# Kernel optimization log

Measured on AMD Instinct MI355X. Metric: run time of the kernel, lower is better.

Reference implementation:

```python
import jax, jax.numpy as jnp
import numpy as np

E, B, S, D, F = 8, 2, 1024, 1024, 4096


def setup_inputs() -> dict:
    key = jax.random.key(0)
    ks = jax.random.split(key, 9)
    sc_d = 1.0 / np.sqrt(D)
    sc_f = 1.0 / np.sqrt(F)
    hidden_states = jax.random.normal(ks[0], (B, S, D), dtype=jnp.float32)
    # router outputs set externally on the parent model in the original code
    gating_probs = jax.nn.softmax(jax.random.normal(ks[1], (B, E), dtype=jnp.float32), axis=-1)
    shared_gate_prob = jax.nn.sigmoid(jax.random.normal(ks[2], (B, 1), dtype=jnp.float32))
    # stacked expert SwiGLU MLP weights (Llama-style gate/up/down)
    Wg = jax.random.normal(ks[3], (E, D, F), dtype=jnp.float32) * sc_d
    Wu = jax.random.normal(ks[4], (E, D, F), dtype=jnp.float32) * sc_d
    Wd = jax.random.normal(ks[5], (E, F, D), dtype=jnp.float32) * sc_f
    # shared expert MLP
    Sg = jax.random.normal(ks[6], (D, F), dtype=jnp.float32) * sc_d
    Su = jax.random.normal(ks[7], (D, F), dtype=jnp.float32) * sc_d
    Sd = jax.random.normal(ks[8], (F, D), dtype=jnp.float32) * sc_f
    return {
        "hidden_states": hidden_states,
        "gating_probs": gating_probs,
        "shared_gate_prob": shared_gate_prob,
        "Wg": Wg, "Wu": Wu, "Wd": Wd,
        "Sg": Sg, "Su": Su, "Sd": Sd,
    }


def reference(hidden_states, gating_probs, shared_gate_prob, Wg, Wu, Wd, Sg, Su, Sd):
    h = hidden_states  # [B,S,D]
    # every expert's MLP runs on all tokens (naive all-experts-dense, as in source)
    g = jnp.einsum("bsd,edf->ebsf", h, Wg)
    u = jnp.einsum("bsd,edf->ebsf", h, Wu)
    expert_outs = jnp.einsum("ebsf,efd->ebsd", jax.nn.silu(g) * u, Wd)  # [E,B,S,D]
    # weighted_sum routing with per-sequence gating probs [B,E]
    expert_output = jnp.einsum("be,ebsd->bsd", gating_probs, expert_outs)
    # shared expert MLP
    shared = jnp.einsum("bsf,fd->bsd", jax.nn.silu(h @ Sg) * (h @ Su), Sd)
    sg = shared_gate_prob[:, :, None]  # [B,1,1]
    return (1.0 - sg) * expert_output + sg * shared
```

## Files before the change

### kernel.cpp

```cpp
#include <hip/hip_runtime.h>
#include <cstdio>
#include <cstdint>

typedef _Float16 f16;
typedef _Float16 f16x4 __attribute__((ext_vector_type(4)));
typedef _Float16 f16x8 __attribute__((ext_vector_type(8)));
typedef float f32x4 __attribute__((ext_vector_type(4)));

#define GLL16(gp, lp)                                                          \
  __builtin_amdgcn_global_load_lds(                                            \
      (const __attribute__((address_space(1))) void*)(gp),                     \
      (__attribute__((address_space(3))) void*)(lp), 16, 0, 0)

#define BARX __builtin_amdgcn_s_barrier()
#define WAITV8 { asm volatile("s_waitcnt vmcnt(8)" ::: "memory"); __builtin_amdgcn_sched_barrier(0); }
#define WAITV4 { asm volatile("s_waitcnt vmcnt(4)" ::: "memory"); __builtin_amdgcn_sched_barrier(0); }
#define WAITV0 { asm volatile("s_waitcnt vmcnt(0)" ::: "memory"); __builtin_amdgcn_sched_barrier(0); }
#define WAITL0 { asm volatile("s_waitcnt lgkmcnt(0)" ::: "memory"); __builtin_amdgcn_sched_barrier(0); }

__global__ void cvt_f32_f16_kernel(const float* __restrict__ in,
                                   f16* __restrict__ out, int n4) {
  int i = blockIdx.x * blockDim.x + threadIdx.x;
  if (i < n4) {
    f32x4 v = reinterpret_cast<const f32x4*>(in)[i];
    f16x4 o;
    o[0] = (f16)v[0]; o[1] = (f16)v[1]; o[2] = (f16)v[2]; o[3] = (f16)v[3];
    reinterpret_cast<f16x4*>(out)[i] = o;
  }
}

__global__ void tr_cvt2_kernel(const float* __restrict__ inA,
                               const float* __restrict__ inB,
                               f16* __restrict__ out, size_t slotOff,
                               int C, size_t OS, int nA) {
  int slot = blockIdx.z;
  const float* src = (slot < nA) ? inA + (size_t)slot * 64 * gridDim.y * C : inB;
  f16* dst = out + (size_t)slot * slotOff;
  __shared__ f16 tl[4096];
  int t = threadIdx.x;
  int r0 = blockIdx.y * 64, c0 = blockIdx.x * 64;
  int br = (t >> 4) * 4, bc = (t & 15) * 4;
  f32x4 v[4];
#pragma unroll
  for (int i = 0; i < 4; ++i)
    v[i] = *(const f32x4*)&src[(size_t)(r0 + br + i) * C + c0 + bc];
#pragma unroll
  for (int cc = 0; cc < 4; ++cc) {
    int c = bc + cc;
    f16x4 o;
    o[0] = (f16)v[0][cc]; o[1] = (f16)v[1][cc];
    o[2] = (f16)v[2][cc]; o[3] = (f16)v[3][cc];
    *(f16x4*)&tl[c * 64 + (br ^ ((c & 7) * 8))] = o;
  }
  __syncthreads();
  int rw = (t & 7) * 8, cw = t >> 3;
#pragma unroll
  for (int j = 0; j < 2; ++j) {
    int c = cw + j * 32;
    f16x8 o = *(const f16x8*)&tl[c * 64 + (rw ^ ((c & 7) * 8))];
    *(f16x8*)&dst[(size_t)(c0 + c) * OS + r0 + rw] = o;
  }
}

#define STG_A4(B)                                                              \
  {                                                                            \
    GLL16(aS, &lds[(B) * 16384 + dA]);                                         \
    GLL16(aS + 131072, &lds[(B) * 16384 + 4096 + dA]);                         \
  }
#define STG_GU4(B)                                                             \
  {                                                                            \
    GLL16(gS, &lds[(B) * 16384 + 8192 + dA]);                                  \
    GLL16(uS, &lds[(B) * 16384 + 12288 + dA]);                                 \
    aS += 32; gS += 32; uS += 32;                                              \
  }

#define RD_G1(B)                                                               \
  do {                                                                         \
    const f16* pa_ = &lds[(B) * 16384 + voffA];                                \
    aF[0] = *(const f16x8*)(pa_);                                              \
    aF[1] = *(const f16x8*)(pa_ + 512);                                        \
    aF[2] = *(const f16x8*)(pa_ + 1024);                                       \
    aF[3] = *(const f16x8*)(pa_ + 1536);                                       \
    const f16* pb_ = &lds[(B) * 16384 + voffB];                                \
    bG[0] = *(const f16x8*)(pb_);                                              \
    bG[1] = *(const f16x8*)(pb_ + 512);                                        \
    bU[0] = *(const f16x8*)(pb_ + 4096);                                       \
    bU[1] = *(const f16x8*)(pb_ + 4608);                                       \
  } while (0)
#define RD_G2(B)                                                               \
  do {                                                                         \
    const f16* pa_ = &lds[(B) * 16384 + voffA + 2048];                         \
    aF[0] = *(const f16x8*)(pa_);                                              \
    aF[1] = *(const f16x8*)(pa_ + 512);                                        \
    aF[2] = *(const f16x8*)(pa_ + 1024);                                       \
    aF[3] = *(const f16x8*)(pa_ + 1536);                                       \
  } while (0)

#define MFMAG(G)                                                               \
  do {                                                                         \
    __builtin_amdgcn_s_setprio(1);                                             \
    _Pragma("unroll") for (int mi = 0; mi < 4; ++mi)                           \
        _Pragma("unroll") for (int ni = 0; ni < 2; ++ni) {                     \
      ag[(G) * 4 + mi][ni] = __builtin_amdgcn_mfma_f32_16x16x32_f16(           \
          aF[mi], bG[ni], ag[(G) * 4 + mi][ni], 0, 0, 0);                      \
      au[(G) * 4 + mi][ni] = __builtin_amdgcn_mfma_f32_16x16x32_f16(           \
          aF[mi], bU[ni], au[(G) * 4 + mi][ni], 0, 0, 0);                      \
    }                                                                          \
    __builtin_amdgcn_s_setprio(0);                                             \
    __builtin_amdgcn_sched_barrier(0);                                         \
  } while (0)

#define KT4(B, DOST, WV)                                                       \
  do {                                                                         \
    RD_G1(B);                                                                  \
    if (DOST) STG_A4(((B) + 3) & 3);                                           \
    BARX; WAITL0; MFMAG(0); BARX;                                              \
    RD_G2(B);                                                                  \
    if (DOST) STG_GU4(((B) + 3) & 3);                                          \
    BARX; WAITL0; MFMAG(1); WV; BARX;                                          \
  } while (0)

__global__ __launch_bounds__(512, 2) void gemmUG4_kernel(
    const f16* __restrict__ A, const f16* __restrict__ Bg,
    const f16* __restrict__ Bu, f16* __restrict__ T,
    const float* __restrict__ gate, const float* __restrict__ sgp) {
  __shared__ __align__(16) f16 lds[65536];

  int lgl = (blockIdx.x & 7) * 288 + (blockIdx.x >> 3);
  int mt = lgl & 7;
  int ntg = lgl >> 3;
  int slot = ntg >> 5;
  int ntl = ntg & 31;

  int t = threadIdx.x, w = t >> 6, l = t & 63;
  int wr = w >> 2, wc = w & 3;

  int arow = t >> 2;
  int aswz = ((t & 3) ^ ((arow >> 1) & 3)) * 8;
  const f16* aS = A + (size_t)(mt * 256 + arow) * 1024 + aswz;
  const f16* gS = Bg + (size_t)slot * 4194304 +
                  (size_t)(ntl * 128 + arow) * 1024 + aswz;
  const f16* uS = Bu + (size_t)slot * 4194304 +
                  (size_t)(ntl * 128 + arow) * 1024 + aswz;
  int dA = t * 8;

  int r15 = l & 15;
  int swz = ((l >> 4) ^ ((r15 >> 1) & 3)) * 8;
  int voffA = wr * 4096 + r15 * 32 + swz;
  int voffB = 8192 + wc * 1024 + r15 * 32 + swz;

  f16x8 aF[4], bG[2], bU[2];
  f32x4 ag[8][2] = {}, au[8][2] = {};

  STG_A4(0); STG_GU4(0);
  STG_A4(1); STG_GU4(1);
  STG_A4(2); STG_GU4(2);
  WAITV8; BARX;

#pragma unroll 1
  for (int it = 0; it < 7; ++it) {
    KT4(0, 1, WAITV8);
    KT4(1, 1, WAITV8);
    KT4(2, 1, WAITV8);
    KT4(3, 1, WAITV8);
  }
  KT4(0, 1, WAITV8);
  KT4(1, 0, WAITV4);
  KT4(2, 0, WAITV0);
  KT4(3, 0, {});

  int r0 = (l >> 4) * 4, c0 = l & 15;
  int rowb = mt * 256 + wr * 128;
  size_t colb = (size_t)ntg * 128 + wc * 32;
  int b = mt >> 2;
  float s = sgp[b];
  float coef = (slot < 8) ? (1.f - s) * gate[b * 8 + slot] : s;
#pragma unroll
  for (int rt = 0; rt < 8; ++rt) {
#pragma unroll
    for (int ni = 0; ni < 2; ++ni) {
#pragma unroll
      for (int j = 0; j < 4; ++j) {
        float g = ag[rt][ni][j];
        float u = au[rt][ni][j];
        T[(size_t)(rowb + rt * 16 + r0 + j) * 36864 + colb + ni * 16 + c0] =
            (f16)(g / (1.f + __expf(-g)) * u * coef);
      }
    }
  }
}

#define STAGE_A(tile, hf)                                                      \
  do {                                                                         \
    const f16* g_ = Abase + (size_t)((hf) * 128) * LD + (tile) * 64 + aVoff;   \
    f16* d_ = &lds[(2 * ((tile) & 1) + (hf)) * 8192 + w * 512];                \
    GLL16(g_, d_);                                                             \
    GLL16(g_ + (size_t)64 * LD, d_ + 4096);                                    \
  } while (0)
#define STAGE_B(tile, hf)                                                      \
  do {                                                                         \
    const f16* g_ = Bbase + (size_t)((hf) * 128) * LD + (tile) * 64 + aVoff;   \
    f16* d_ = &lds[32768 + (2 * ((tile) & 1) + (hf)) * 8192 + w * 512];        \
    GLL16(g_, d_);                                                             \
    GLL16(g_ + (size_t)64 * LD, d_ + 4096);                                    \
  } while (0)

#define RD_A(rh, buf)                                                          \
  do {                                                                         \
    const f16* p_ = &lds[(2 * (buf) + wr) * 8192 + (rh) * 4096];               \
    aFd[0][0] = *(const f16x8*)(p_ + 0 * 1024 + vR0);                          \
    aFd[0][1] = *(const f16x8*)(p_ + 0 * 1024 + vR1);                          \
    aFd[1][0] = *(const f16x8*)(p_ + 1 * 1024 + vR0);                          \
    aFd[1][1] = *(const f16x8*)(p_ + 1 * 1024 + vR1);                          \
    aFd[2][0] = *(const f16x8*)(p_ + 2 * 1024 + vR0);                          \
    aFd[2][1] = *(const f16x8*)(p_ + 2 * 1024 + vR1);                          \
    aFd[3][0] = *(const f16x8*)(p_ + 3 * 1024 + vR0);                          \
    aFd[3][1] = *(const f16x8*)(p_ + 3 * 1024 + vR1);                          \
  } while (0)
#define RD_B(ch, buf)                                                          \
  do {                                                                         \
    const f16* p_ = &lds[32768 + (2 * (buf) + bh) * 8192 + bq * 4096 +         \
                         (ch) * 2 * 1024];                                     \
    bFd[(ch) * 2][0] = *(const f16x8*)(p_ + vR0);                              \
    bFd[(ch) * 2][1] = *(const f16x8*)(p_ + vR1);                              \
    bFd[(ch) * 2 + 1][0] = *(const f16x8*)(p_ + 1024 + vR0);                   \
    bFd[(ch) * 2 + 1][1] = *(const f16x8*)(p_ + 1024 + vR1);                   \
  } while (0)

#define MFMA16(rh, ch)                                                         \
  do {                                                                         \
    __builtin_amdgcn_s_setprio(1);                                             \
    _Pragma("unroll") for (int rt = 0; rt < 4; ++rt)                           \
        _Pragma("unroll") for (int ct = 0; ct < 2; ++ct)                       \
        _Pragma("unroll") for (int ks = 0; ks < 2; ++ks)                       \
            acc[(rh) * 4 + rt][(ch) * 2 + ct] =                                \
        __builtin_amdgcn_mfma_f32_16x16x32_f16(                                \
            aFd[rt][ks], bFd[(ch) * 2 + ct][ks],                               \
            acc[(rh) * 4 + rt][(ch) * 2 + ct], 0, 0, 0);                       \
    __builtin_amdgcn_s_setprio(0);                                             \
    __builtin_amdgcn_sched_barrier(0);                                         \
  } while (0)

__global__ __launch_bounds__(512, 2) void gemmD_kernel(
    const f16* __restrict__ A, const f16* __restrict__ B,
    float* __restrict__ P) {
  constexpr size_t LD = 36864;
  constexpr int NTILES = 72;
  __shared__ __align__(16) f16 lds[65536];

  int wg = (blockIdx.x & 7) * 32 + (blockIdx.x >> 3);
  int kpart = wg >> 5, mt = (wg >> 2) & 7, nt = wg & 3;

  int t = threadIdx.x, w = t >> 6, l = t & 63;
  int wr = w >> 2, wc = w & 3;
  int bh = wc >> 1, bq = wc & 1;

  int scol = (((l & 7) ^ ((l >> 3) & 7)) * 8);
  size_t stRow = (size_t)(w * 8 + (l >> 3)) * LD;
  size_t aVoff = stRow + scol;
  const f16* Abase = A + (size_t)mt * 256 * LD + (size_t)kpart * 4608;
  const f16* Bbase = B + (size_t)nt * 256 * LD + (size_t)kpart * 4608;

  int vR0 = (l & 15) * 64 + (((l >> 4) * 8) ^ ((l & 7) * 8));
  int vR1 = (l & 15) * 64 + ((32 + (l >> 4) * 8) ^ ((l & 7) * 8));

  f16x8 aFd[4][2], bFd[4][2];
  f32x4 acc[8][4] = {};

  STAGE_B(0, 0); STAGE_B(0, 1);
  STAGE_A(0, 0); STAGE_A(0, 1);
  STAGE_B(1, 0); STAGE_B(1, 1);
  WAITV4;
  BARX;

#pragma unroll 1
  for (int it = 0; it < NTILES / 2 - 1; ++it) {
    int t1 = 2 * it + 1, t2 = 2 * it + 2, t3 = 2 * it + 3;
    RD_A(0, 0); RD_B(0, 0); STAGE_A(t1, 0);
    BARX; WAITL0; MFMA16(0, 0); BARX;
    RD_B(1, 0); STAGE_A(t1, 1);
    BARX; WAITL0; MFMA16(0, 1); BARX;
    RD_A(1, 0); STAGE_B(t2, 0);
    BARX; WAITL0; MFMA16(1, 0); BARX;
    STAGE_B(t2, 1);
    BARX; MFMA16(1, 1); WAITV4; BARX;
    RD_A(0, 1); RD_B(0, 1); STAGE_A(t2, 0);
    BARX; WAITL0; MFMA16(0, 0); BARX;
    RD_B(1, 1); STAGE_A(t2, 1);
    BARX; WAITL0; MFMA16(0, 1); BARX;
    RD_A(1, 1); STAGE_B(t3, 0);
    BARX; WAITL0; MFMA16(1, 0); BARX;
    STAGE_B(t3, 1);
    BARX; MFMA16(1, 1); WAITV4; BARX;
  }
  RD_A(0, 0); RD_B(0, 0); STAGE_A(NTILES - 1, 0);
  BARX; WAITL0; MFMA16(0, 0); BARX;
  RD_B(1, 0); STAGE_A(NTILES - 1, 1);
  BARX; WAITL0; MFMA16(0, 1); BARX;
  RD_A(1, 0);
  BARX; WAITL0; MFMA16(1, 0); BARX;
  BARX; MFMA16(1, 1); WAITV0; BARX;
  RD_A(0, 1); RD_B(0, 1);
  BARX; WAITL0; MFMA16(0, 0); BARX;
  RD_B(1, 1);
  BARX; WAITL0; MFMA16(0, 1); BARX;
  RD_A(1, 1);
  BARX; WAITL0; MFMA16(1, 0); BARX;
  MFMA16(1, 1);

  int r0 = (l >> 4) * 4, c0 = l & 15;
  size_t base = ((size_t)kpart << 21);
  int rowbase = mt * 256 + wr * 128;
  int colbase = nt * 256 + wc * 64;
#pragma unroll
  for (int rt = 0; rt < 8; ++rt)
#pragma unroll
    for (int ct = 0; ct < 4; ++ct)
#pragma unroll
      for (int j = 0; j < 4; ++j)
        P[base + (size_t)(rowbase + rt * 16 + r0 + j) * 1024 + colbase +
          ct * 16 + c0] = acc[rt][ct][j];
}

__global__ void reduce8_kernel(const float* __restrict__ P,
                               float* __restrict__ out, int n4) {
  int i = blockIdx.x * blockDim.x + threadIdx.x;
  if (i < n4) {
    f32x4 s = {0.f, 0.f, 0.f, 0.f};
#pragma unroll
    for (int e = 0; e < 8; ++e) {
      f32x4 v = reinterpret_cast<const f32x4*>(P + ((size_t)e << 21))[i];
      s += v;
    }
    reinterpret_cast<f32x4*>(out)[i] = s;
  }
}

extern "C" void kernel_launch(void* const* d_in, const int* in_sizes, int n_in,
                              void* d_out, int out_size, void* d_ws,
                              size_t ws_size, hipStream_t stream) {
  const float* h    = (const float*)d_in[0];
  const float* gate = (const float*)d_in[1];
  const float* sgp  = (const float*)d_in[2];
  const float* Wg   = (const float*)d_in[3];
  const float* Wu   = (const float*)d_in[4];
  const float* Wd   = (const float*)d_in[5];
  const float* Sg   = (const float*)d_in[6];
  const float* Su   = (const float*)d_in[7];
  const float* Sd   = (const float*)d_in[8];

  const size_t SZ_HB = 4194304;
  const size_t SZ_W  = 75497472;
  const size_t SZ_T  = 150994944;
  const size_t SZ_P  = 67108864;
  char* ws = (char*)d_ws;
  f16*   hb  = (f16*)(ws);
  f16*   WgT = (f16*)(ws + SZ_HB);
  f16*   WuT = (f16*)(ws + SZ_HB + SZ_W);
  f16*   WdT = (f16*)(ws + SZ_HB + 2 * SZ_W);
  f16*   T   = (f16*)(ws + SZ_HB + 3 * SZ_W);
  float* P   = (float*)(ws + SZ_HB + 3 * SZ_W + SZ_T);
  size_t need = SZ_HB + 3 * SZ_W + SZ_T + SZ_P;
  if (ws_size < need) {
    fprintf(stderr, "kernel_launch: ws too small (%zu < %zu)\n", ws_size, need);
    return;
  }
  float* out = (float*)d_out;

  cvt_f32_f16_kernel<<<2048, 256, 0, stream>>>(h, hb, 524288);
  tr_cvt2_kernel<<<dim3(64, 16, 9), 256, 0, stream>>>(
      Wg, Sg, WgT, 4096ull * 1024, 4096, 1024, 8);
  tr_cvt2_kernel<<<dim3(64, 16, 9), 256, 0, stream>>>(
      Wu, Su, WuT, 4096ull * 1024, 4096, 1024, 8);
  tr_cvt2_kernel<<<dim3(16, 64, 9), 256, 0, stream>>>(
      Wd, Sd, WdT, 4096, 1024, 36864, 8);

  gemmUG4_kernel<<<2304, 512, 0, stream>>>(hb, WgT, WuT, T, gate, sgp);
  gemmD_kernel<<<256, 512, 0, stream>>>(T, WdT, P);
  reduce8_kernel<<<2048, 256, 0, stream>>>(P, out, 524288);
}
```

Before: 582.7 us.

## Restructure gate/up GEMM as single 256x256 tile with LDS-exchanged SwiGLU epilogue

The gate/up GEMM now treats the gate and up weight tiles as one 256-wide B operand. Each wave computes a 128x64 region with K=64 double-buffered tiles instead of interleaved gate/up fragments with K=32 quad buffering. Waves that hold up results write them to LDS so the gate-holding waves can apply SiLU, the gating coefficient and the store. This aims to improve MFMA operand reuse and cut LDS fragment reads per MFMA. The cost is an extra LDS exchange and barrier in the epilogue, and only half the waves doing the final stores.

```diff
diff --git a/kernel.cpp b/kernel.cpp
--- a/kernel.cpp
+++ b/kernel.cpp
@@ -13,7 +13,6 @@
       (__attribute__((address_space(3))) void*)(lp), 16, 0, 0)
 
 #define BARX __builtin_amdgcn_s_barrier()
-#define WAITV8 { asm volatile("s_waitcnt vmcnt(8)" ::: "memory"); __builtin_amdgcn_sched_barrier(0); }
 #define WAITV4 { asm volatile("s_waitcnt vmcnt(4)" ::: "memory"); __builtin_amdgcn_sched_barrier(0); }
 #define WAITV0 { asm volatile("s_waitcnt vmcnt(0)" ::: "memory"); __builtin_amdgcn_sched_barrier(0); }
 #define WAITL0 { asm volatile("s_waitcnt lgkmcnt(0)" ::: "memory"); __builtin_amdgcn_sched_barrier(0); }
@@ -62,65 +61,65 @@
   }
 }
 
-#define STG_A4(B)                                                              \
-  {                                                                            \
-    GLL16(aS, &lds[(B) * 16384 + dA]);                                         \
-    GLL16(aS + 131072, &lds[(B) * 16384 + 4096 + dA]);                         \
-  }
-#define STG_GU4(B)                                                             \
-  {                                                                            \
-    GLL16(gS, &lds[(B) * 16384 + 8192 + dA]);                                  \
-    GLL16(uS, &lds[(B) * 16384 + 12288 + dA]);                                 \
-    aS += 32; gS += 32; uS += 32;                                              \
-  }
-
-#define RD_G1(B)                                                               \
-  do {                                                                         \
-    const f16* pa_ = &lds[(B) * 16384 + voffA];                                \
-    aF[0] = *(const f16x8*)(pa_);                                              \
-    aF[1] = *(const f16x8*)(pa_ + 512);                                        \
-    aF[2] = *(const f16x8*)(pa_ + 1024);                                       \
-    aF[3] = *(const f16x8*)(pa_ + 1536);                                       \
-    const f16* pb_ = &lds[(B) * 16384 + voffB];                                \
-    bG[0] = *(const f16x8*)(pb_);                                              \
-    bG[1] = *(const f16x8*)(pb_ + 512);                                        \
-    bU[0] = *(const f16x8*)(pb_ + 4096);                                       \
-    bU[1] = *(const f16x8*)(pb_ + 4608);                                       \
-  } while (0)
-#define RD_G2(B)                                                               \
-  do {                                                                         \
-    const f16* pa_ = &lds[(B) * 16384 + voffA + 2048];                         \
-    aF[0] = *(const f16x8*)(pa_);                                              \
-    aF[1] = *(const f16x8*)(pa_ + 512);                                        \
-    aF[2] = *(const f16x8*)(pa_ + 1024);                                       \
-    aF[3] = *(const f16x8*)(pa_ + 1536);                                       \
-  } while (0)
-
-#define MFMAG(G)                                                               \
+#define STAGE_A5(tile, hf)                                                     \
+  do {                                                                         \
+    const f16* g_ = Abase + (size_t)((hf) * 128) * 1024 + (tile) * 64 + aVoff; \
+    f16* d_ = &lds[(2 * ((tile) & 1) + (hf)) * 8192 + w * 512];                \
+    GLL16(g_, d_);                                                             \
+    GLL16(g_ + (size_t)64 * 1024, d_ + 4096);                                  \
+  } while (0)
+#define STAGE_G5(tile)                                                         \
+  do {                                                                         \
+    const f16* g_ = Gbase + (tile) * 64 + aVoff;                               \
+    f16* d_ = &lds[32768 + (2 * ((tile) & 1)) * 8192 + w * 512];               \
+    GLL16(g_, d_);                                                             \
+    GLL16(g_ + (size_t)64 * 1024, d_ + 4096);                                  \
+  } while (0)
+#define STAGE_U5(tile)                                                         \
+  do {                                                                         \
+    const f16* g_ = Ubase + (tile) * 64 + aVoff;                               \
+    f16* d_ = &lds[32768 + (2 * ((tile) & 1) + 1) * 8192 + w * 512];           \
+    GLL16(g_, d_);                                                             \
+    GLL16(g_ + (size_t)64 * 1024, d_ + 4096);                                  \
+  } while (0)
+
+#define RD_A5(rh, buf)                                                         \
+  do {                                                                         \
+    const f16* p_ = &lds[(2 * (buf) + wr) * 8192 + (rh) * 4096];               \
+    aFd[0][0] = *(const f16x8*)(p_ + 0 * 1024 + vR0);                          \
+    aFd[0][1] = *(const f16x8*)(p_ + 0 * 1024 + vR1);                          \
+    aFd[1][0] = *(const f16x8*)(p_ + 1 * 1024 + vR0);                          \
+    aFd[1][1] = *(const f16x8*)(p_ + 1 * 1024 + vR1);                          \
+    aFd[2][0] = *(const f16x8*)(p_ + 2 * 1024 + vR0);                          \
+    aFd[2][1] = *(const f16x8*)(p_ + 2 * 1024 + vR1);                          \
+    aFd[3][0] = *(const f16x8*)(p_ + 3 * 1024 + vR0);                          \
+    aFd[3][1] = *(const f16x8*)(p_ + 3 * 1024 + vR1);                          \
+  } while (0)
+#define RD_B5(ch, buf)                                                         \
+  do {                                                                         \
+    const f16* p_ = &lds[32768 + (2 * (buf) + bh) * 8192 + bq * 4096 +         \
+                         (ch) * 2 * 1024];                                     \
+    bFd[(ch) * 2][0] = *(const f16x8*)(p_ + vR0);                              \
+    bFd[(ch) * 2][1] = *(const f16x8*)(p_ + vR1);                              \
+    bFd[(ch) * 2 + 1][0] = *(const f16x8*)(p_ + 1024 + vR0);                   \
+    bFd[(ch) * 2 + 1][1] = *(const f16x8*)(p_ + 1024 + vR1);                   \
+  } while (0)
+
+#define MFMA165(rh, ch)                                                        \
   do {                                                                         \
     __builtin_amdgcn_s_setprio(1);                                             \
-    _Pragma("unroll") for (int mi = 0; mi < 4; ++mi)                           \
-        _Pragma("unroll") for (int ni = 0; ni < 2; ++ni) {                     \
-      ag[(G) * 4 + mi][ni] = __builtin_amdgcn_mfma_f32_16x16x32_f16(           \
-          aF[mi], bG[ni], ag[(G) * 4 + mi][ni], 0, 0, 0);                      \
-      au[(G) * 4 + mi][ni] = __builtin_amdgcn_mfma_f32_16x16x32_f16(           \
-          aF[mi], bU[ni], au[(G) * 4 + mi][ni], 0, 0, 0);                      \
-    }                                                                          \
+    _Pragma("unroll") for (int rt = 0; rt < 4; ++rt)                           \
+        _Pragma("unroll") for (int ct = 0; ct < 2; ++ct)                       \
+        _Pragma("unroll") for (int ks = 0; ks < 2; ++ks)                       \
+            acc[(rh) * 4 + rt][(ch) * 2 + ct] =                                \
+        __builtin_amdgcn_mfma_f32_16x16x32_f16(                                \
+            aFd[rt][ks], bFd[(ch) * 2 + ct][ks],                               \
+            acc[(rh) * 4 + rt][(ch) * 2 + ct], 0, 0, 0);                       \
     __builtin_amdgcn_s_setprio(0);                                             \
     __builtin_amdgcn_sched_barrier(0);                                         \
   } while (0)
 
-#define KT4(B, DOST, WV)                                                       \
-  do {                                                                         \
-    RD_G1(B);                                                                  \
-    if (DOST) STG_A4(((B) + 3) & 3);                                           \
-    BARX; WAITL0; MFMAG(0); BARX;                                              \
-    RD_G2(B);                                                                  \
-    if (DOST) STG_GU4(((B) + 3) & 3);                                          \
-    BARX; WAITL0; MFMAG(1); WV; BARX;                                          \
-  } while (0)
-
-__global__ __launch_bounds__(512, 2) void gemmUG4_kernel(
+__global__ __launch_bounds__(512, 2) void gemmUG5_kernel(
     const f16* __restrict__ A, const f16* __restrict__ Bg,
     const f16* __restrict__ Bu, f16* __restrict__ T,
     const float* __restrict__ gate, const float* __restrict__ sgp) {
@@ -134,57 +133,92 @@
 
   int t = threadIdx.x, w = t >> 6, l = t & 63;
   int wr = w >> 2, wc = w & 3;
-
-  int arow = t >> 2;
-  int aswz = ((t & 3) ^ ((arow >> 1) & 3)) * 8;
-  const f16* aS = A + (size_t)(mt * 256 + arow) * 1024 + aswz;
-  const f16* gS = Bg + (size_t)slot * 4194304 +
-                  (size_t)(ntl * 128 + arow) * 1024 + aswz;
-  const f16* uS = Bu + (size_t)slot * 4194304 +
-                  (size_t)(ntl * 128 + arow) * 1024 + aswz;
-  int dA = t * 8;
-
-  int r15 = l & 15;
-  int swz = ((l >> 4) ^ ((r15 >> 1) & 3)) * 8;
-  int voffA = wr * 4096 + r15 * 32 + swz;
-  int voffB = 8192 + wc * 1024 + r15 * 32 + swz;
-
-  f16x8 aF[4], bG[2], bU[2];
-  f32x4 ag[8][2] = {}, au[8][2] = {};
-
-  STG_A4(0); STG_GU4(0);
-  STG_A4(1); STG_GU4(1);
-  STG_A4(2); STG_GU4(2);
-  WAITV8; BARX;
+  int bh = wc >> 1, bq = wc & 1;
+
+  int scol = (((l & 7) ^ ((l >> 3) & 7)) * 8);
+  size_t aVoff = (size_t)(w * 8 + (l >> 3)) * 1024 + scol;
+  const f16* Abase = A + (size_t)mt * 256 * 1024;
+  const f16* Gbase = Bg + (size_t)slot * 4194304 + (size_t)ntl * 128 * 1024;
+  const f16* Ubase = Bu + (size_t)slot * 4194304 + (size_t)ntl * 128 * 1024;
+
+  int vR0 = (l & 15) * 64 + (((l >> 4) * 8) ^ ((l & 7) * 8));
+  int vR1 = (l & 15) * 64 + ((32 + (l >> 4) * 8) ^ ((l & 7) * 8));
+
+  f16x8 aFd[4][2], bFd[4][2];
+  f32x4 acc[8][4] = {};
+
+  STAGE_G5(0); STAGE_U5(0);
+  STAGE_A5(0, 0); STAGE_A5(0, 1);
+  STAGE_G5(1); STAGE_U5(1);
+  WAITV4;
+  BARX;
 
 #pragma unroll 1
   for (int it = 0; it < 7; ++it) {
-    KT4(0, 1, WAITV8);
-    KT4(1, 1, WAITV8);
-    KT4(2, 1, WAITV8);
-    KT4(3, 1, WAITV8);
-  }
-  KT4(0, 1, WAITV8);
-  KT4(1, 0, WAITV4);
-  KT4(2, 0, WAITV0);
-  KT4(3, 0, {});
+    int t1 = 2 * it + 1, t2 = 2 * it + 2, t3 = 2 * it + 3;
+    RD_A5(0, 0); RD_B5(0, 0); STAGE_A5(t1, 0);
+    BARX; WAITL0; MFMA165(0, 0); BARX;
+    RD_B5(1, 0); STAGE_A5(t1, 1);
+    BARX; WAITL0; MFMA165(0, 1); BARX;
+    RD_A5(1, 0); STAGE_G5(t2);
+    BARX; WAITL0; MFMA165(1, 0); BARX;
+    STAGE_U5(t2);
+    BARX; MFMA165(1, 1); WAITV4; BARX;
+    RD_A5(0, 1); RD_B5(0, 1); STAGE_A5(t2, 0);
+    BARX; WAITL0; MFMA165(0, 0); BARX;
+    RD_B5(1, 1); STAGE_A5(t2, 1);
+    BARX; WAITL0; MFMA165(0, 1); BARX;
+    RD_A5(1, 1); STAGE_G5(t3);
+    BARX; WAITL0; MFMA165(1, 0); BARX;
+    STAGE_U5(t3);
+    BARX; MFMA165(1, 1); WAITV4; BARX;
+  }
+  RD_A5(0, 0); RD_B5(0, 0); STAGE_A5(15, 0);
+  BARX; WAITL0; MFMA165(0, 0); BARX;
+  RD_B5(1, 0); STAGE_A5(15, 1);
+  BARX; WAITL0; MFMA165(0, 1); BARX;
+  RD_A5(1, 0);
+  BARX; WAITL0; MFMA165(1, 0); BARX;
+  BARX; MFMA165(1, 1); WAITV0; BARX;
+  RD_A5(0, 1); RD_B5(0, 1);
+  BARX; WAITL0; MFMA165(0, 0); BARX;
+  RD_B5(1, 1);
+  BARX; WAITL0; MFMA165(0, 1); BARX;
+  RD_A5(1, 1);
+  BARX; WAITL0; MFMA165(1, 0); BARX;
+  MFMA165(1, 1);
 
   int r0 = (l >> 4) * 4, c0 = l & 15;
-  int rowb = mt * 256 + wr * 128;
-  size_t colb = (size_t)ntg * 128 + wc * 32;
-  int b = mt >> 2;
-  float s = sgp[b];
-  float coef = (slot < 8) ? (1.f - s) * gate[b * 8 + slot] : s;
-#pragma unroll
-  for (int rt = 0; rt < 8; ++rt) {
-#pragma unroll
-    for (int ni = 0; ni < 2; ++ni) {
-#pragma unroll
-      for (int j = 0; j < 4; ++j) {
-        float g = ag[rt][ni][j];
-        float u = au[rt][ni][j];
-        T[(size_t)(rowb + rt * 16 + r0 + j) * 36864 + colb + ni * 16 + c0] =
-            (f16)(g / (1.f + __expf(-g)) * u * coef);
+  float* xf = (float*)lds;
+  if (wc >= 2) {
+    float* wb = xf + (wr * 2 + (wc - 2)) * 8192 + l * 128;
+#pragma unroll
+    for (int rt = 0; rt < 8; ++rt)
+#pragma unroll
+      for (int ct = 0; ct < 4; ++ct)
+        *(f32x4*)(wb + ((rt ^ (l & 7)) * 16 + ct * 4)) = acc[rt][ct];
+  }
+  WAITL0;
+  BARX;
+  if (wc < 2) {
+    const float* rb = xf + (wr * 2 + wc) * 8192 + l * 128;
+    int rowb = mt * 256 + wr * 128;
+    size_t colb = (size_t)ntg * 128 + wc * 64;
+    int b = mt >> 2;
+    float s = sgp[b];
+    float coef = (slot < 8) ? (1.f - s) * gate[b * 8 + slot] : s;
+#pragma unroll
+    for (int rt = 0; rt < 8; ++rt) {
+#pragma unroll
+      for (int ct = 0; ct < 4; ++ct) {
+        f32x4 uv = *(const f32x4*)(rb + ((rt ^ (l & 7)) * 16 + ct * 4));
+#pragma unroll
+        for (int j = 0; j < 4; ++j) {
+          float g = acc[rt][ct][j];
+          float u = uv[j];
+          T[(size_t)(rowb + rt * 16 + r0 + j) * 36864 + colb + ct * 16 + c0] =
+              (f16)(g / (1.f + __expf(-g)) * u * coef);
+        }
       }
     }
   }
@@ -375,7 +409,7 @@
   tr_cvt2_kernel<<<dim3(16, 64, 9), 256, 0, stream>>>(
       Wd, Sd, WdT, 4096, 1024, 36864, 8);
 
-  gemmUG4_kernel<<<2304, 512, 0, stream>>>(hb, WgT, WuT, T, gate, sgp);
+  gemmUG5_kernel<<<2304, 512, 0, stream>>>(hb, WgT, WuT, T, gate, sgp);
   gemmD_kernel<<<256, 512, 0, stream>>>(T, WdT, P);
   reduce8_kernel<<<2048, 256, 0, stream>>>(P, out, 524288);
 }
```

Measured after the change: 613.7 us. 5.3% more time.

## Make gate/up GEMM persistent over 9 tiles and store split-K partials in fp16

Applied to the files above, without the earlier changes.

The gate/up GEMM kernel now launches 256 persistent workgroups, each looping over 9 consecutive N-tiles. It prefetches the next tile's operands during the tail of the current tile, so the pipeline prologue and epilogue are paid once per workgroup instead of once per tile. Separately, the down-projection split-K partials are stored as fp16 instead of fp32, halving partial-buffer traffic in gemmD and the reduce kernel. The risks are lower precision in the partial sums and a tail imbalance, since 256 workgroups may not evenly fill the CUs.

```diff
diff --git a/kernel.cpp b/kernel.cpp
--- a/kernel.cpp
+++ b/kernel.cpp
@@ -120,28 +120,27 @@
     BARX; WAITL0; MFMAG(1); WV; BARX;                                          \
   } while (0)
 
-__global__ __launch_bounds__(512, 2) void gemmUG4_kernel(
+__global__ __launch_bounds__(512, 2) void gemmUG6_kernel(
     const f16* __restrict__ A, const f16* __restrict__ Bg,
     const f16* __restrict__ Bu, f16* __restrict__ T,
     const float* __restrict__ gate, const float* __restrict__ sgp) {
   __shared__ __align__(16) f16 lds[65536];
 
-  int lgl = (blockIdx.x & 7) * 288 + (blockIdx.x >> 3);
-  int mt = lgl & 7;
-  int ntg = lgl >> 3;
-  int slot = ntg >> 5;
-  int ntl = ntg & 31;
+  int mt = blockIdx.x & 7;
+  int q = blockIdx.x >> 3;
 
   int t = threadIdx.x, w = t >> 6, l = t & 63;
   int wr = w >> 2, wc = w & 3;
 
   int arow = t >> 2;
   int aswz = ((t & 3) ^ ((arow >> 1) & 3)) * 8;
-  const f16* aS = A + (size_t)(mt * 256 + arow) * 1024 + aswz;
-  const f16* gS = Bg + (size_t)slot * 4194304 +
-                  (size_t)(ntl * 128 + arow) * 1024 + aswz;
-  const f16* uS = Bu + (size_t)slot * 4194304 +
-                  (size_t)(ntl * 128 + arow) * 1024 + aswz;
+  const f16* aS0 = A + (size_t)(mt * 256 + arow) * 1024 + aswz;
+  const f16* aS = aS0;
+  int ntg0 = q * 9;
+  const f16* gS = Bg + (size_t)(ntg0 >> 5) * 4194304 +
+                  (size_t)((ntg0 & 31) * 128 + arow) * 1024 + aswz;
+  const f16* uS = Bu + (size_t)(ntg0 >> 5) * 4194304 +
+                  (size_t)((ntg0 & 31) * 128 + arow) * 1024 + aswz;
   int dA = t * 8;
 
   int r15 = l & 15;
@@ -152,39 +151,59 @@
   f16x8 aF[4], bG[2], bU[2];
   f32x4 ag[8][2] = {}, au[8][2] = {};
 
+  int r0 = (l >> 4) * 4, c0 = l & 15;
+  int rowb = mt * 256 + wr * 128;
+  float sgv = sgp[mt >> 2];
+
   STG_A4(0); STG_GU4(0);
   STG_A4(1); STG_GU4(1);
   STG_A4(2); STG_GU4(2);
   WAITV8; BARX;
 
 #pragma unroll 1
-  for (int it = 0; it < 7; ++it) {
+  for (int s = 0; s < 9; ++s) {
+    int ntg = q * 9 + s;
+    int slot = ntg >> 5;
+
+#pragma unroll 1
+    for (int it = 0; it < 7; ++it) {
+      KT4(0, 1, WAITV8);
+      KT4(1, 1, WAITV8);
+      KT4(2, 1, WAITV8);
+      KT4(3, 1, WAITV8);
+    }
     KT4(0, 1, WAITV8);
-    KT4(1, 1, WAITV8);
-    KT4(2, 1, WAITV8);
-    KT4(3, 1, WAITV8);
-  }
-  KT4(0, 1, WAITV8);
-  KT4(1, 0, WAITV4);
-  KT4(2, 0, WAITV0);
-  KT4(3, 0, {});
-
-  int r0 = (l >> 4) * 4, c0 = l & 15;
-  int rowb = mt * 256 + wr * 128;
-  size_t colb = (size_t)ntg * 128 + wc * 32;
-  int b = mt >> 2;
-  float s = sgp[b];
-  float coef = (slot < 8) ? (1.f - s) * gate[b * 8 + slot] : s;
-#pragma unroll
-  for (int rt = 0; rt < 8; ++rt) {
-#pragma unroll
-    for (int ni = 0; ni < 2; ++ni) {
-#pragma unroll
-      for (int j = 0; j < 4; ++j) {
-        float g = ag[rt][ni][j];
-        float u = au[rt][ni][j];
-        T[(size_t)(rowb + rt * 16 + r0 + j) * 36864 + colb + ni * 16 + c0] =
-            (f16)(g / (1.f + __expf(-g)) * u * coef);
+    if (s < 8) {
+      aS -= 1024;
+      int ntg2 = ntg + 1;
+      gS = Bg + (size_t)(ntg2 >> 5) * 4194304 +
+           (size_t)((ntg2 & 31) * 128 + arow) * 1024 + aswz;
+      uS = Bu + (size_t)(ntg2 >> 5) * 4194304 +
+           (size_t)((ntg2 & 31) * 128 + arow) * 1024 + aswz;
+      KT4(1, 1, WAITV8);
+      KT4(2, 1, WAITV8);
+      KT4(3, 1, WAITV8);
+    } else {
+      KT4(1, 0, WAITV4);
+      KT4(2, 0, WAITV0);
+      KT4(3, 0, {});
+    }
+
+    size_t colb = (size_t)ntg * 128 + wc * 32;
+    float coef = (slot < 8) ? (1.f - sgv) * gate[(mt >> 2) * 8 + slot] : sgv;
+#pragma unroll
+    for (int rt = 0; rt < 8; ++rt) {
+#pragma unroll
+      for (int ni = 0; ni < 2; ++ni) {
+#pragma unroll
+        for (int j = 0; j < 4; ++j) {
+          float g = ag[rt][ni][j];
+          float u = au[rt][ni][j];
+          T[(size_t)(rowb + rt * 16 + r0 + j) * 36864 + colb + ni * 16 + c0] =
+              (f16)(g / (1.f + __expf(-g)) * u * coef);
+        }
+        ag[rt][ni] = (f32x4){0.f, 0.f, 0.f, 0.f};
+        au[rt][ni] = (f32x4){0.f, 0.f, 0.f, 0.f};
       }
     }
   }
@@ -243,7 +262,7 @@
 
 __global__ __launch_bounds__(512, 2) void gemmD_kernel(
     const f16* __restrict__ A, const f16* __restrict__ B,
-    float* __restrict__ P) {
+    f16* __restrict__ P) {
   constexpr size_t LD = 36864;
   constexpr int NTILES = 72;
   __shared__ __align__(16) f16 lds[65536];
@@ -319,18 +338,19 @@
 #pragma unroll
       for (int j = 0; j < 4; ++j)
         P[base + (size_t)(rowbase + rt * 16 + r0 + j) * 1024 + colbase +
-          ct * 16 + c0] = acc[rt][ct][j];
-}
-
-__global__ void reduce8_kernel(const float* __restrict__ P,
+          ct * 16 + c0] = (f16)acc[rt][ct][j];
+}
+
+__global__ void reduce8_kernel(const f16* __restrict__ P,
                                float* __restrict__ out, int n4) {
   int i = blockIdx.x * blockDim.x + threadIdx.x;
   if (i < n4) {
     f32x4 s = {0.f, 0.f, 0.f, 0.f};
 #pragma unroll
     for (int e = 0; e < 8; ++e) {
-      f32x4 v = reinterpret_cast<const f32x4*>(P + ((size_t)e << 21))[i];
-      s += v;
+      f16x4 v = reinterpret_cast<const f16x4*>(P + ((size_t)e << 21))[i];
+      s[0] += (float)v[0]; s[1] += (float)v[1];
+      s[2] += (float)v[2]; s[3] += (float)v[3];
     }
     reinterpret_cast<f32x4*>(out)[i] = s;
   }
@@ -352,14 +372,14 @@
   const size_t SZ_HB = 4194304;
   const size_t SZ_W  = 75497472;
   const size_t SZ_T  = 150994944;
-  const size_t SZ_P  = 67108864;
+  const size_t SZ_P  = 33554432;
   char* ws = (char*)d_ws;
   f16*   hb  = (f16*)(ws);
   f16*   WgT = (f16*)(ws + SZ_HB);
   f16*   WuT = (f16*)(ws + SZ_HB + SZ_W);
   f16*   WdT = (f16*)(ws + SZ_HB + 2 * SZ_W);
   f16*   T   = (f16*)(ws + SZ_HB + 3 * SZ_W);
-  float* P   = (float*)(ws + SZ_HB + 3 * SZ_W + SZ_T);
+  f16*   P   = (f16*)(ws + SZ_HB + 3 * SZ_W + SZ_T);
   size_t need = SZ_HB + 3 * SZ_W + SZ_T + SZ_P;
   if (ws_size < need) {
     fprintf(stderr, "kernel_launch: ws too small (%zu < %zu)\n", ws_size, need);
@@ -375,7 +395,7 @@
   tr_cvt2_kernel<<<dim3(16, 64, 9), 256, 0, stream>>>(
       Wd, Sd, WdT, 4096, 1024, 36864, 8);
 
-  gemmUG4_kernel<<<2304, 512, 0, stream>>>(hb, WgT, WuT, T, gate, sgp);
+  gemmUG6_kernel<<<256, 512, 0, stream>>>(hb, WgT, WuT, T, gate, sgp);
   gemmD_kernel<<<256, 512, 0, stream>>>(T, WdT, P);
   reduce8_kernel<<<2048, 256, 0, stream>>>(P, out, 524288);
 }
```

New measurement: 688.7 us. 18.2% more time.
